# Performance work log

Measured on AMD Instinct MI355X. Metric: run time of the kernel, lower is better.

## Reference

```python
import jax, jax.numpy as jnp
import numpy as np

N = 50000          # nodes
E = 800000         # edges (before self-loops)
F_IN, F_HID, F_OUT = 128, 64, 64
NEG_SLOPE_ATT = 0.2   # GATConv internal leaky_relu
NEG_SLOPE_ACT = 0.01  # F.leaky_relu default between layers


def setup_inputs() -> dict:
    key = jax.random.key(0)
    ks = jax.random.split(key, 16)

    def glorot(k, shape):
        fan = float(sum(shape)) if len(shape) > 1 else float(shape[0])
        return jax.random.normal(k, shape, jnp.float32) * (2.0 / fan) ** 0.5

    return {
        "x": jax.random.normal(ks[0], (N, F_IN), jnp.float32),
        "edge_index": jax.random.randint(ks[1], (2, E), 0, N, dtype=jnp.int64),
        "W1": glorot(ks[2], (F_IN, F_HID)),
        "a_src1": glorot(ks[3], (F_HID,)),
        "a_dst1": glorot(ks[4], (F_HID,)),
        "b1": jnp.zeros((F_HID,), jnp.float32),
        "W2": glorot(ks[5], (F_HID, F_HID)),
        "a_src2": glorot(ks[6], (F_HID,)),
        "a_dst2": glorot(ks[7], (F_HID,)),
        "b2": jnp.zeros((F_HID,), jnp.float32),
        "W3": glorot(ks[8], (F_HID, F_OUT)),
        "a_src3": glorot(ks[9], (F_OUT,)),
        "a_dst3": glorot(ks[10], (F_OUT,)),
        "b3": jnp.zeros((F_OUT,), jnp.float32),
    }


def gat_conv(h, src, dst, W, a_src, a_dst, b):
    # Single-head PyG GATConv: project, per-edge scores, segment softmax over dst, scatter-add.
    z = h @ W                              # [N, C]
    e_src = z @ a_src                      # [N]
    e_dst = z @ a_dst                      # [N]
    e = jax.nn.leaky_relu(e_src[src] + e_dst[dst], NEG_SLOPE_ATT)  # [E']
    m = jax.ops.segment_max(e, dst, num_segments=N)
    ex = jnp.exp(e - m[dst])
    denom = jax.ops.segment_sum(ex, dst, num_segments=N)
    alpha = ex / (denom[dst] + 1e-16)      # segment softmax (PyG adds 1e-16)
    out = jax.ops.segment_sum(alpha[:, None] * z[src], dst, num_segments=N) + b
    return out, alpha


def reference(x, edge_index, W1, a_src1, a_dst1, b1, W2, a_src2, a_dst2, b2, W3, a_src3, a_dst3, b3):
    # add_self_loops=True (GATConv default): append (i, i) for every node
    loops = jnp.arange(N, dtype=edge_index.dtype)
    ei = jnp.concatenate([edge_index, jnp.stack([loops, loops])], axis=1)  # [2, E+N]
    src, dst = ei[0], ei[1]

    h = x
    alpha = None
    for (W, asr, ads, b) in ((W1, a_src1, a_dst1, b1),
                             (W2, a_src2, a_dst2, b2),
                             (W3, a_src3, a_dst3, b3)):
        h, alpha = gat_conv(h, src, dst, W, asr, ads, b)
        h = jax.nn.leaky_relu(h, NEG_SLOPE_ACT)
    return (h, ei, alpha)
```

## Files before the change

kernel.cpp:

```cpp
#include <hip/hip_runtime.h>
#include <hip/hip_bf16.h>
#include <hip/hip_fp8.h>

#define NN 50000
#define EE 800000
#define E2 850000
#define F_IN 128
#define F_HID 64
#define NCHUNK ((NN + 255) / 256)
#define NTILE  ((NN + 63) / 64)
#define AGGB 2048
#define SLICES 512
#define SCHUNK ((E2 + SLICES - 1) / SLICES)

__device__ __forceinline__ unsigned char f32_to_fp8(float x) {
    __hip_fp8_e4m3 t(x);
    return t.__x;
}
__device__ __forceinline__ float fp8_to_f32(unsigned char b) {
    __hip_fp8_e4m3 t; t.__x = b;
    return (float)t;
}

#if defined(__has_builtin)
#  if __has_builtin(__builtin_amdgcn_cvt_f32_fp8)
#    define CVT_FP8(v, s) __builtin_amdgcn_cvt_f32_fp8((v), (s))
#  endif
#endif
#ifndef CVT_FP8
#  define CVT_FP8(v, s) fp8_to_f32(((v) >> (8 * (s))) & 255)
#endif

__global__ __launch_bounds__(256) void hist_ei_kernel(const int* __restrict__ ei,
                                                      int* __restrict__ deg,
                                                      float* __restrict__ ei_out) {
    int e = blockIdx.x * 256 + threadIdx.x;
    if (e >= E2) return;
    int s, d;
    if (e < EE) { s = ei[e]; d = ei[EE + e]; }
    else        { s = d = e - EE; }
    atomicAdd(&deg[d], 1);
    ei_out[e]      = (float)s;
    ei_out[E2 + e] = (float)d;
}

__global__ __launch_bounds__(256) void scan_part12(const int* __restrict__ deg,
                                                   int* __restrict__ csum,
                                                   int* __restrict__ ticket) {
    int i = blockIdx.x * 256 + threadIdx.x;
    int v = (i < NN) ? deg[i] : 0;
#pragma unroll
    for (int d = 32; d; d >>= 1) v += __shfl_xor(v, d);
    __shared__ int ws[4];
    if ((threadIdx.x & 63) == 0) ws[threadIdx.x >> 6] = v;
    __syncthreads();
    __shared__ int isLast;
    if (threadIdx.x == 0) {
        atomicExch(&csum[blockIdx.x], ws[0] + ws[1] + ws[2] + ws[3]);
        __threadfence();
        isLast = (atomicAdd(ticket, 1) == gridDim.x - 1) ? 1 : 0;
    }
    __syncthreads();
    if (isLast) {
        __threadfence();
        __shared__ int sd[256];
        int t = threadIdx.x;
        int v2 = (t < NCHUNK) ? atomicAdd(&csum[t], 0) : 0;
        sd[t] = v2;
        __syncthreads();
        for (int off = 1; off < 256; off <<= 1) {
            int o = (t >= off) ? sd[t - off] : 0;
            __syncthreads();
            sd[t] += o;
            __syncthreads();
        }
        if (t < NCHUNK) atomicExch(&csum[t], sd[t] - v2);
    }
}

__global__ __launch_bounds__(256) void scan_part3(const int* __restrict__ deg,
                                                  const int* __restrict__ csum,
                                                  int* __restrict__ offs,
                                                  int* __restrict__ cursor) {
    __shared__ int sd[256];
    int t = threadIdx.x;
    int i = blockIdx.x * 256 + t;
    int v = (i < NN) ? deg[i] : 0;
    sd[t] = v;
    __syncthreads();
    for (int off = 1; off < 256; off <<= 1) {
        int o = (t >= off) ? sd[t - off] : 0;
        __syncthreads();
        sd[t] += o;
        __syncthreads();
    }
    if (i < NN) {
        int ex = sd[t] - v + csum[blockIdx.x];
        offs[i] = ex;
        cursor[i] = ex;
    }
}

__global__ __launch_bounds__(256) void scatter_kernel(const int* __restrict__ ei,
                                                      int* __restrict__ cursor,
                                                      int* __restrict__ src_sorted) {
    int g = blockIdx.x & 7;
    int slice = blockIdx.x >> 3;
    int begin = slice * SCHUNK;
    int end = begin + SCHUNK; if (end > E2) end = E2;
    for (int e = begin + threadIdx.x; e < end; e += 256) {
        int s, d;
        if (e < EE) { s = ei[e]; d = ei[EE + e]; }
        else        { s = d = e - EE; }
        int bucket = (d * 8) / NN;
        if (bucket == g) {
            int pos = atomicAdd(&cursor[d], 1);
            src_sorted[pos] = s;
        }
    }
}

template <int K>
__global__ __launch_bounds__(256) void gemm_tile(const float* __restrict__ h,
                                                 const float* __restrict__ W,
                                                 const float* __restrict__ a_src,
                                                 const float* __restrict__ a_dst,
                                                 unsigned char* __restrict__ z8,
                                                 float* __restrict__ es,
                                                 float* __restrict__ ed) {
    constexpr int LDA = K + 4;
    __shared__ float Alds[64 * LDA];
    __shared__ float Blds[K * 64];

    int tid = threadIdx.x;
    int base = blockIdx.x * 64;

    {
        constexpr int F4R = K / 4;
        for (int t = tid; t < 64 * F4R; t += 256) {
            int r = t / F4R;
            int c4 = t % F4R;
            int gr = base + r;
            if (gr >= NN) gr = NN - 1;
            float4 v = *(const float4*)(h + (size_t)gr * K + c4 * 4);
            *(float4*)(&Alds[r * LDA + c4 * 4]) = v;
        }
    }
    for (int t = tid; t < K * 16; t += 256) {
        float4 v = *(const float4*)(W + t * 4);
        *(float4*)(&Blds[t * 4]) = v;
    }
    __syncthreads();

    int tx = tid & 15;
    int ty = tid >> 4;

    float acc[4][4] = {};
#pragma unroll 4
    for (int k = 0; k < K; k += 4) {
        float4 a[4], b[4];
#pragma unroll
        for (int i = 0; i < 4; ++i)
            a[i] = *(const float4*)(&Alds[(4 * ty + i) * LDA + k]);
#pragma unroll
        for (int kk = 0; kk < 4; ++kk)
            b[kk] = *(const float4*)(&Blds[(k + kk) * 64 + 4 * tx]);
#pragma unroll
        for (int i = 0; i < 4; ++i) {
            acc[i][0] = fmaf(a[i].x, b[0].x, acc[i][0]);
            acc[i][1] = fmaf(a[i].x, b[0].y, acc[i][1]);
            acc[i][2] = fmaf(a[i].x, b[0].z, acc[i][2]);
            acc[i][3] = fmaf(a[i].x, b[0].w, acc[i][3]);
            acc[i][0] = fmaf(a[i].y, b[1].x, acc[i][0]);
            acc[i][1] = fmaf(a[i].y, b[1].y, acc[i][1]);
            acc[i][2] = fmaf(a[i].y, b[1].z, acc[i][2]);
            acc[i][3] = fmaf(a[i].y, b[1].w, acc[i][3]);
            acc[i][0] = fmaf(a[i].z, b[2].x, acc[i][0]);
            acc[i][1] = fmaf(a[i].z, b[2].y, acc[i][1]);
            acc[i][2] = fmaf(a[i].z, b[2].z, acc[i][2]);
            acc[i][3] = fmaf(a[i].z, b[2].w, acc[i][3]);
            acc[i][0] = fmaf(a[i].w, b[3].x, acc[i][0]);
            acc[i][1] = fmaf(a[i].w, b[3].y, acc[i][1]);
            acc[i][2] = fmaf(a[i].w, b[3].z, acc[i][2]);
            acc[i][3] = fmaf(a[i].w, b[3].w, acc[i][3]);
        }
    }

    float4 as4 = *(const float4*)(a_src + 4 * tx);
    float4 ad4 = *(const float4*)(a_dst + 4 * tx);
    float ps[4], pd[4];
#pragma unroll
    for (int i = 0; i < 4; ++i) {
        int gr = base + 4 * ty + i;
        if (gr < NN) {
            unsigned int pk = (unsigned int)f32_to_fp8(acc[i][0])
                            | ((unsigned int)f32_to_fp8(acc[i][1]) << 8)
                            | ((unsigned int)f32_to_fp8(acc[i][2]) << 16)
                            | ((unsigned int)f32_to_fp8(acc[i][3]) << 24);
            *(unsigned int*)(&z8[(size_t)gr * 64 + 4 * tx]) = pk;
        }
        ps[i] = acc[i][0] * as4.x + acc[i][1] * as4.y + acc[i][2] * as4.z + acc[i][3] * as4.w;
        pd[i] = acc[i][0] * ad4.x + acc[i][1] * ad4.y + acc[i][2] * ad4.z + acc[i][3] * ad4.w;
    }
#pragma unroll
    for (int d = 1; d < 16; d <<= 1) {
#pragma unroll
        for (int i = 0; i < 4; ++i) {
            ps[i] += __shfl_xor(ps[i], d);
            pd[i] += __shfl_xor(pd[i], d);
        }
    }
    if (tx == 0) {
#pragma unroll
        for (int i = 0; i < 4; ++i) {
            int gr = base + 4 * ty + i;
            if (gr < NN) { es[gr] = ps[i]; ed[gr] = pd[i]; }
        }
    }
}

__global__ __launch_bounds__(256) void aggregate(const int* __restrict__ offs,
                                                 const int* __restrict__ deg,
                                                 const int* __restrict__ src_sorted,
                                                 const float* __restrict__ es,
                                                 const float* __restrict__ ed,
                                                 const unsigned char* __restrict__ z8,
                                                 const float* __restrict__ bias,
                                                 float* __restrict__ hout,
                                                 float* __restrict__ denom_out) {
    int tid = threadIdx.x;
    int lane = tid & 63;
    int wave = blockIdx.x * 4 + (tid >> 6);
    const int NW = AGGB * 4;

    int sub  = lane >> 4;
    int fgrp = (lane & 15) * 4;
    const unsigned char* zp = z8 + fgrp;
    float4 bi4 = *(const float4*)(bias + fgrp);

    int n = wave;
    if (n >= NN) return;
    n = __builtin_amdgcn_readfirstlane(n);
    int off = offs[n];
    int dg = deg[n];
    float edn = ed[n];
    int sv = src_sorted[off + ((lane < dg) ? lane : 0)];
    float ese = es[sv];

    while (true) {
        int n2 = n + NW;
        bool more = (n2 < NN);
        int off2 = 0, dg2 = 0; float edn2 = 0.f;
        if (more) {
            n2 = __builtin_amdgcn_readfirstlane(n2);
            off2 = offs[n2]; dg2 = deg[n2]; edn2 = ed[n2];
        }

        float dsum = 0.f;
        float a0 = 0.f, a1 = 0.f, a2 = 0.f, a3 = 0.f;
        for (int b0 = 0; b0 < dg; b0 += 64) {
            int bl = dg - b0; if (bl > 64) bl = 64;
            int svb; float esv;
            if (b0 == 0) { svb = sv; esv = ese; }
            else {
                svb = src_sorted[off + b0 + ((lane < bl) ? lane : 0)];
                esv = es[svb];
            }
            float e = esv + edn;
            e = (e > 0.f) ? e : 0.2f * e;
            float w = (lane < bl) ? __expf(e) : 0.f;
            dsum += w;

            int ng = (bl + 3) >> 2;
            int j = 0;
            for (; j + 4 <= ng; j += 4) {
                int i0 = 4 * j + sub;
                int   s0 = __shfl(svb, i0);
                int   s1 = __shfl(svb, i0 + 4);
                int   s2 = __shfl(svb, i0 + 8);
                int   s3 = __shfl(svb, i0 + 12);
                unsigned int v0 = *(const unsigned int*)(zp + (size_t)s0 * 64);
                unsigned int v1 = *(const unsigned int*)(zp + (size_t)s1 * 64);
                unsigned int v2 = *(const unsigned int*)(zp + (size_t)s2 * 64);
                unsigned int v3 = *(const unsigned int*)(zp + (size_t)s3 * 64);
                float w0 = __shfl(w, i0);
                float w1 = __shfl(w, i0 + 4);
                float w2 = __shfl(w, i0 + 8);
                float w3 = __shfl(w, i0 + 12);
                a0 = fmaf(w0, CVT_FP8(v0, 0), a0);
                a1 = fmaf(w0, CVT_FP8(v0, 1), a1);
                a2 = fmaf(w0, CVT_FP8(v0, 2), a2);
                a3 = fmaf(w0, CVT_FP8(v0, 3), a3);
                a0 = fmaf(w1, CVT_FP8(v1, 0), a0);
                a1 = fmaf(w1, CVT_FP8(v1, 1), a1);
                a2 = fmaf(w1, CVT_FP8(v1, 2), a2);
                a3 = fmaf(w1, CVT_FP8(v1, 3), a3);
                a0 = fmaf(w2, CVT_FP8(v2, 0), a0);
                a1 = fmaf(w2, CVT_FP8(v2, 1), a1);
                a2 = fmaf(w2, CVT_FP8(v2, 2), a2);
                a3 = fmaf(w2, CVT_FP8(v2, 3), a3);
                a0 = fmaf(w3, CVT_FP8(v3, 0), a0);
                a1 = fmaf(w3, CVT_FP8(v3, 1), a1);
                a2 = fmaf(w3, CVT_FP8(v3, 2), a2);
                a3 = fmaf(w3, CVT_FP8(v3, 3), a3);
            }
            for (; j < ng; ++j) {
                int i0 = 4 * j + sub;
                int   s0 = __shfl(svb, i0);
                unsigned int v0 = *(const unsigned int*)(zp + (size_t)s0 * 64);
                float w0 = __shfl(w, i0);
                a0 = fmaf(w0, CVT_FP8(v0, 0), a0);
                a1 = fmaf(w0, CVT_FP8(v0, 1), a1);
                a2 = fmaf(w0, CVT_FP8(v0, 2), a2);
                a3 = fmaf(w0, CVT_FP8(v0, 3), a3);
            }
        }

        int sv2 = 0;
        if (more) sv2 = src_sorted[off2 + ((lane < dg2) ? lane : 0)];

        a0 += __shfl_xor(a0, 16); a1 += __shfl_xor(a1, 16);
        a2 += __shfl_xor(a2, 16); a3 += __shfl_xor(a3, 16);
        a0 += __shfl_xor(a0, 32); a1 += __shfl_xor(a1, 32);
        a2 += __shfl_xor(a2, 32); a3 += __shfl_xor(a3, 32);
#pragma unroll
        for (int d = 32; d; d >>= 1) dsum += __shfl_xor(dsum, d);

        float ese2 = 0.f;
        if (more) ese2 = es[sv2];

        float inv = 1.f / (dsum + 1e-16f);
        if (lane < 16) {
            float4 o;
            o.x = a0 * inv + bi4.x;
            o.y = a1 * inv + bi4.y;
            o.z = a2 * inv + bi4.z;
            o.w = a3 * inv + bi4.w;
            o.x = (o.x > 0.f) ? o.x : 0.01f * o.x;
            o.y = (o.y > 0.f) ? o.y : 0.01f * o.y;
            o.z = (o.z > 0.f) ? o.z : 0.01f * o.z;
            o.w = (o.w > 0.f) ? o.w : 0.01f * o.w;
            *(float4*)(hout + (size_t)n * 64 + fgrp) = o;
        }
        if (lane == 0) denom_out[n] = dsum;

        if (!more) break;
        n = n2; off = off2; dg = dg2; edn = edn2; sv = sv2; ese = ese2;
    }
}

__global__ __launch_bounds__(256) void alpha_kernel(const int* __restrict__ ei,
                                                    const float* __restrict__ es,
                                                    const float* __restrict__ ed,
                                                    const float* __restrict__ denom,
                                                    float* __restrict__ alpha_out) {
    int e = blockIdx.x * 256 + threadIdx.x;
    if (e >= E2) return;
    int s, d;
    if (e < EE) { s = ei[e]; d = ei[EE + e]; }
    else        { s = d = e - EE; }
    float x = es[s] + ed[d];
    x = (x > 0.f) ? x : 0.2f * x;
    alpha_out[e] = __expf(x) / (denom[d] + 1e-16f);
}

extern "C" void kernel_launch(void* const* d_in, const int* in_sizes, int n_in,
                              void* d_out, int out_size, void* d_ws, size_t ws_size,
                              hipStream_t stream) {
    const float* x   = (const float*)d_in[0];
    const int*   ei  = (const int*)d_in[1];
    const float* W1  = (const float*)d_in[2];
    const float* as1 = (const float*)d_in[3];
    const float* ad1 = (const float*)d_in[4];
    const float* b1  = (const float*)d_in[5];
    const float* W2  = (const float*)d_in[6];
    const float* as2 = (const float*)d_in[7];
    const float* ad2 = (const float*)d_in[8];
    const float* b2  = (const float*)d_in[9];
    const float* W3  = (const float*)d_in[10];
    const float* as3 = (const float*)d_in[11];
    const float* ad3 = (const float*)d_in[12];
    const float* b3  = (const float*)d_in[13];

    float* out       = (float*)d_out;
    float* h_out     = out;
    float* ei_out    = out + (size_t)NN * 64;
    float* alpha_out = ei_out + 2 * (size_t)E2;

    char* w = (char*)d_ws;
    auto carve = [&](size_t bytes) {
        void* p = (void*)w;
        w += (bytes + 255) & ~size_t(255);
        return p;
    };
    float* h1  = (float*)carve((size_t)NN * 64 * 4);
    float* h2  = (float*)carve((size_t)NN * 64 * 4);
    unsigned char* z8 = (unsigned char*)carve((size_t)NN * 64);
    float* es  = (float*)carve((size_t)NN * 4);
    float* ed  = (float*)carve((size_t)NN * 4);
    float* denom = (float*)carve((size_t)NN * 4);
    int* deg        = (int*)carve(((size_t)NN + 64) * 4);
    int* ticket     = deg + NN;
    int* offs       = (int*)carve((size_t)NN * 4);
    int* cursor     = (int*)carve((size_t)NN * 4);
    int* csum       = (int*)carve((size_t)NCHUNK * 4);
    int* src_sorted = (int*)carve((size_t)E2 * 4);

    const int EB = (E2 + 255) / 256;

    hipMemsetAsync(deg, 0, ((size_t)NN + 64) * 4, stream);
    hist_ei_kernel<<<EB, 256, 0, stream>>>(ei, deg, ei_out);
    scan_part12<<<NCHUNK, 256, 0, stream>>>(deg, csum, ticket);
    scan_part3<<<NCHUNK, 256, 0, stream>>>(deg, csum, offs, cursor);
    scatter_kernel<<<SLICES * 8, 256, 0, stream>>>(ei, cursor, src_sorted);

    gemm_tile<F_IN><<<NTILE, 256, 0, stream>>>(x, W1, as1, ad1, z8, es, ed);
    aggregate<<<AGGB, 256, 0, stream>>>(offs, deg, src_sorted, es, ed, z8, b1, h1, denom);
    gemm_tile<F_HID><<<NTILE, 256, 0, stream>>>(h1, W2, as2, ad2, z8, es, ed);
    aggregate<<<AGGB, 256, 0, stream>>>(offs, deg, src_sorted, es, ed, z8, b2, h2, denom);
    gemm_tile<F_HID><<<NTILE, 256, 0, stream>>>(h2, W3, as3, ad3, z8, es, ed);
    aggregate<<<AGGB, 256, 0, stream>>>(offs, deg, src_sorted, es, ed, z8, b3, h_out, denom);
    alpha_kernel<<<EB, 256, 0, stream>>>(ei, es, ed, denom, alpha_out);
}
```

Before: 304.2 us.

## Partition edges into destination bins during histogram, then scatter from bins

```diff
diff --git a/kernel.cpp b/kernel.cpp
--- a/kernel.cpp
+++ b/kernel.cpp
@@ -10,8 +10,13 @@
 #define NCHUNK ((NN + 255) / 256)
 #define NTILE  ((NN + 63) / 64)
 #define AGGB 2048
-#define SLICES 512
-#define SCHUNK ((E2 + SLICES - 1) / SLICES)
+
+#define PNB 32
+#define BCAP 32768
+#define PCAP 128
+#define PCHUNK 2048
+#define PBLOCKS ((EE + PCHUNK - 1) / PCHUNK)
+#define SLICEB 64
 
 __device__ __forceinline__ unsigned char f32_to_fp8(float x) {
     __hip_fp8_e4m3 t(x);
@@ -31,24 +36,56 @@
 #  define CVT_FP8(v, s) fp8_to_f32(((v) >> (8 * (s))) & 255)
 #endif
 
-__global__ __launch_bounds__(256) void hist_ei_kernel(const int* __restrict__ ei,
-                                                      int* __restrict__ deg,
-                                                      float* __restrict__ ei_out) {
-    int e = blockIdx.x * 256 + threadIdx.x;
-    if (e >= E2) return;
-    int s, d;
-    if (e < EE) { s = ei[e]; d = ei[EE + e]; }
-    else        { s = d = e - EE; }
-    atomicAdd(&deg[d], 1);
-    ei_out[e]      = (float)s;
-    ei_out[E2 + e] = (float)d;
+__global__ __launch_bounds__(256) void hist_part_kernel(const int* __restrict__ ei,
+                                                        int* __restrict__ deg,
+                                                        int* __restrict__ bin_cur,
+                                                        unsigned long long* __restrict__ bins,
+                                                        float* __restrict__ ei_out) {
+    __shared__ unsigned long long buf[PNB * PCAP];
+    __shared__ int cnt[PNB];
+    __shared__ int basep[PNB];
+    int tid = threadIdx.x;
+    if (tid < PNB) cnt[tid] = 0;
+    __syncthreads();
+
+    int e0 = blockIdx.x * PCHUNK;
+    int eend = e0 + PCHUNK; if (eend > EE) eend = EE;
+    for (int e = e0 + tid; e < eend; e += 256) {
+        int s = ei[e], d = ei[EE + e];
+        atomicAdd(&deg[d], 1);
+        ei_out[e]      = (float)s;
+        ei_out[E2 + e] = (float)d;
+        int b = (int)(((long long)d * PNB) / NN);
+        unsigned long long pk = ((unsigned long long)(unsigned)d << 32) | (unsigned)s;
+        int r = atomicAdd(&cnt[b], 1);
+        if (r < PCAP) buf[b * PCAP + r] = pk;
+        else {
+            int p = atomicAdd(&bin_cur[b], 1);
+            if (p < BCAP) bins[(size_t)b * BCAP + p] = pk;
+        }
+    }
+    __syncthreads();
+    if (tid < PNB) {
+        int c = cnt[tid]; if (c > PCAP) c = PCAP;
+        basep[tid] = c ? atomicAdd(&bin_cur[tid], c) : 0;
+        cnt[tid] = c;
+    }
+    __syncthreads();
+    for (int b = 0; b < PNB; ++b) {
+        int c = cnt[b];
+        int bb = basep[b];
+        for (int i = tid; i < c; i += 256) {
+            int p = bb + i;
+            if (p < BCAP) bins[(size_t)b * BCAP + p] = buf[b * PCAP + i];
+        }
+    }
 }
 
 __global__ __launch_bounds__(256) void scan_part12(const int* __restrict__ deg,
                                                    int* __restrict__ csum,
                                                    int* __restrict__ ticket) {
     int i = blockIdx.x * 256 + threadIdx.x;
-    int v = (i < NN) ? deg[i] : 0;
+    int v = (i < NN) ? deg[i] + 1 : 0;
 #pragma unroll
     for (int d = 32; d; d >>= 1) v += __shfl_xor(v, d);
     __shared__ int ws[4];
@@ -81,11 +118,13 @@
 __global__ __launch_bounds__(256) void scan_part3(const int* __restrict__ deg,
                                                   const int* __restrict__ csum,
                                                   int* __restrict__ offs,
-                                                  int* __restrict__ cursor) {
+                                                  int* __restrict__ cursor,
+                                                  int* __restrict__ src_sorted,
+                                                  float* __restrict__ ei_out) {
     __shared__ int sd[256];
     int t = threadIdx.x;
     int i = blockIdx.x * 256 + t;
-    int v = (i < NN) ? deg[i] : 0;
+    int v = (i < NN) ? deg[i] + 1 : 0;
     sd[t] = v;
     __syncthreads();
     for (int off = 1; off < 256; off <<= 1) {
@@ -97,26 +136,28 @@
     if (i < NN) {
         int ex = sd[t] - v + csum[blockIdx.x];
         offs[i] = ex;
-        cursor[i] = ex;
-    }
-}
-
-__global__ __launch_bounds__(256) void scatter_kernel(const int* __restrict__ ei,
-                                                      int* __restrict__ cursor,
-                                                      int* __restrict__ src_sorted) {
-    int g = blockIdx.x & 7;
-    int slice = blockIdx.x >> 3;
-    int begin = slice * SCHUNK;
-    int end = begin + SCHUNK; if (end > E2) end = E2;
-    for (int e = begin + threadIdx.x; e < end; e += 256) {
-        int s, d;
-        if (e < EE) { s = ei[e]; d = ei[EE + e]; }
-        else        { s = d = e - EE; }
-        int bucket = (d * 8) / NN;
-        if (bucket == g) {
-            int pos = atomicAdd(&cursor[d], 1);
-            src_sorted[pos] = s;
-        }
+        cursor[i] = ex + 1;
+        src_sorted[ex] = i;
+        ei_out[EE + i]      = (float)i;
+        ei_out[E2 + EE + i] = (float)i;
+    }
+}
+
+__global__ __launch_bounds__(256) void scatter_bins(const int* __restrict__ bin_cur,
+                                                    const unsigned long long* __restrict__ bins,
+                                                    int* __restrict__ cursor,
+                                                    int* __restrict__ src_sorted) {
+    int b = blockIdx.x & (PNB - 1);
+    int slice = blockIdx.x >> 5;
+    int cnt = bin_cur[b];
+    if (cnt > BCAP) cnt = BCAP;
+    const unsigned long long* bp = bins + (size_t)b * BCAP;
+    for (int i = slice * 256 + threadIdx.x; i < cnt; i += SLICEB * 256) {
+        unsigned long long v = bp[i];
+        int d = (int)(v >> 32);
+        int s = (int)(v & 0xffffffffu);
+        int pos = atomicAdd(&cursor[d], 1);
+        src_sorted[pos] = s;
     }
 }
 
@@ -242,7 +283,7 @@
     if (n >= NN) return;
     n = __builtin_amdgcn_readfirstlane(n);
     int off = offs[n];
-    int dg = deg[n];
+    int dg = deg[n] + 1;
     float edn = ed[n];
     int sv = src_sorted[off + ((lane < dg) ? lane : 0)];
     float ese = es[sv];
@@ -253,7 +294,7 @@
         int off2 = 0, dg2 = 0; float edn2 = 0.f;
         if (more) {
             n2 = __builtin_amdgcn_readfirstlane(n2);
-            off2 = offs[n2]; dg2 = deg[n2]; edn2 = ed[n2];
+            off2 = offs[n2]; dg2 = deg[n2] + 1; edn2 = ed[n2];
         }
 
         float dsum = 0.f;
@@ -401,18 +442,20 @@
     float* denom = (float*)carve((size_t)NN * 4);
     int* deg        = (int*)carve(((size_t)NN + 64) * 4);
     int* ticket     = deg + NN;
+    int* bin_cur    = deg + NN + 1;
     int* offs       = (int*)carve((size_t)NN * 4);
     int* cursor     = (int*)carve((size_t)NN * 4);
     int* csum       = (int*)carve((size_t)NCHUNK * 4);
     int* src_sorted = (int*)carve((size_t)E2 * 4);
+    unsigned long long* bins = (unsigned long long*)carve((size_t)PNB * BCAP * 8);
 
     const int EB = (E2 + 255) / 256;
 
     hipMemsetAsync(deg, 0, ((size_t)NN + 64) * 4, stream);
-    hist_ei_kernel<<<EB, 256, 0, stream>>>(ei, deg, ei_out);
+    hist_part_kernel<<<PBLOCKS, 256, 0, stream>>>(ei, deg, bin_cur, bins, ei_out);
     scan_part12<<<NCHUNK, 256, 0, stream>>>(deg, csum, ticket);
-    scan_part3<<<NCHUNK, 256, 0, stream>>>(deg, csum, offs, cursor);
-    scatter_kernel<<<SLICES * 8, 256, 0, stream>>>(ei, cursor, src_sorted);
+    scan_part3<<<NCHUNK, 256, 0, stream>>>(deg, csum, offs, cursor, src_sorted, ei_out);
+    scatter_bins<<<PNB * SLICEB, 256, 0, stream>>>(bin_cur, bins, cursor, src_sorted);
 
     gemm_tile<F_IN><<<NTILE, 256, 0, stream>>>(x, W1, as1, ad1, z8, es, ed);
     aggregate<<<AGGB, 256, 0, stream>>>(offs, deg, src_sorted, es, ed, z8, b1, h1, denom);
```

Measured after the change: 305.6 us. No clear change (+0.5%).
